# Kernel optimization log

Measured on AMD Instinct MI355X. Metric: run time of the kernel, lower is better.

## Reference

```python
import jax, jax.numpy as jnp
import numpy as np
from math import factorial

LMAX = 4
N_COEFF = (LMAX + 1) ** 2      # 25 real spherical-harmonic coefficients
N_RADII = 300                  # distance_bins
N_NODES = 512
FEAT = 128
RES_BETA, RES_ALPHA = 180, 360
DIST_STEP = 0.05


def _sh_basis(lmax, y, alpha):
    """Real spherical harmonics evaluated on a (beta, alpha) product grid.
    y = cos(beta) quadrature nodes. Returns [res_beta, res_alpha, (lmax+1)^2]."""
    B, A = len(y), len(alpha)
    P = np.zeros((lmax + 1, lmax + 1, B))
    P[0, 0] = 1.0
    s = np.sqrt(np.clip(1.0 - y * y, 0.0, None))
    for m in range(1, lmax + 1):
        P[m, m] = -(2 * m - 1) * s * P[m - 1, m - 1]
    for m in range(lmax):
        P[m + 1, m] = (2 * m + 1) * y * P[m, m]
    for m in range(lmax + 1):
        for l in range(m + 2, lmax + 1):
            P[l, m] = ((2 * l - 1) * y * P[l - 1, m] - (l + m - 1) * P[l - 2, m]) / (l - m)
    cols = []
    for l in range(lmax + 1):
        for m in range(-l, l + 1):
            am = abs(m)
            Nlm = np.sqrt((2 * l + 1) / (4 * np.pi) * factorial(l - am) / factorial(l + am))
            if m == 0:
                col = Nlm * P[l, 0][:, None] * np.ones((1, A))
            elif m > 0:
                col = np.sqrt(2.0) * Nlm * P[l, m][:, None] * np.cos(m * alpha)[None, :]
            else:
                col = np.sqrt(2.0) * Nlm * P[l, am][:, None] * np.sin(am * alpha)[None, :]
            cols.append(col)
    return np.stack(cols, axis=-1).astype(np.float32)


def setup_inputs() -> dict:
    key = jax.random.key(0)
    ks = jax.random.split(key, 14)

    def lin(k, a, b):
        return jax.random.normal(k, (a, b), jnp.float32) / np.float32(np.sqrt(a))

    x = jax.random.normal(ks[0], (N_NODES, FEAT), jnp.float32)
    fd = [FEAT, 128, 128, 64, 16, 2]
    td = [FEAT, 128, 128, 128, 128, 128, 6]
    fW = [lin(ks[1 + i], fd[i], fd[i + 1]) for i in range(5)]
    tW = [lin(ks[6 + i], td[i], td[i + 1]) for i in range(6)]
    pos_w = lin(ks[12], 2 * FEAT, N_RADII * N_COEFF)
    type_emb = jax.random.normal(ks[13], (5, FEAT), jnp.float32)

    y_np, w_np = np.polynomial.legendre.leggauss(RES_BETA)
    alpha_np = np.linspace(0.0, 2.0 * np.pi, RES_ALPHA, endpoint=False)
    basis = jnp.asarray(_sh_basis(LMAX, y_np, alpha_np))          # [B, A, C]
    qw = jnp.asarray(w_np / 2.0, jnp.float32)                     # gausslegendre / 2
    y_grid = jnp.asarray(y_np, jnp.float32)
    alpha_grid = jnp.asarray(alpha_np, jnp.float32)

    return {
        "x": x,
        "focus_w1": fW[0], "focus_w2": fW[1], "focus_w3": fW[2], "focus_w4": fW[3], "focus_w5": fW[4],
        "type_w1": tW[0], "type_w2": tW[1], "type_w3": tW[2], "type_w4": tW[3], "type_w5": tW[4], "type_w6": tW[5],
        "pos_w": pos_w, "type_emb": type_emb,
        "basis": basis, "qw": qw, "y_grid": y_grid, "alpha_grid": alpha_grid,
        "res_beta": RES_BETA, "res_alpha": RES_ALPHA,
    }


def reference(x, focus_w1, focus_w2, focus_w3, focus_w4, focus_w5,
              type_w1, type_w2, type_w3, type_w4, type_w5, type_w6,
              pos_w, type_emb, basis, qw, y_grid, alpha_grid,
              res_beta, res_alpha):
    n_nodes = x.shape[0]

    # --- focus MLP (relu), per-node logits; STOP logit 0 appended ---
    h = x
    for W in (focus_w1, focus_w2, focus_w3, focus_w4):
        h = jax.nn.relu(h @ W)
    focus_scores = (h @ focus_w5)[:, 0]                             # [n_nodes]
    focus_probs = jax.nn.softmax(jnp.concatenate([focus_scores, jnp.zeros((1,), x.dtype)]))
    focus = jnp.minimum(jnp.argmax(focus_probs), n_nodes - 1)

    # --- type MLP (softplus) on the focus node's features ---
    feat_f = x[focus]                                               # [128]
    th = feat_f
    for W in (type_w1, type_w2, type_w3, type_w4, type_w5):
        th = jax.nn.softplus(th @ W)
    type_dist = jax.nn.softmax(th @ type_w6)                        # [6]
    type_idx = jnp.minimum(jnp.argmax(type_dist), 4)

    # --- position head: SH coefficients per radial shell ---
    pos_in = jnp.concatenate([feat_f, type_emb[type_idx]])          # [256]
    coeffs = (pos_in @ pos_w).reshape(N_RADII, N_COEFF)             # [R, C]

    # to_s2grid: log-density on the sphere for every radial shell
    f = jnp.einsum('rc,bac->rba', coeffs, basis)                    # [R, B, A]
    log_meas = jnp.log(qw)[:, None] + jnp.log(2.0 * jnp.pi / res_alpha)  # [B, 1]

    # radial distribution: integral of exp(f) over the sphere, per shell
    log_radial = jax.nn.logsumexp(f + log_meas[None], axis=(1, 2))  # [R]
    radial_probs = jax.nn.softmax(log_radial)

    key = jax.random.key(42)
    k_r, k_a = jax.random.split(key)
    r_idx = jax.random.categorical(k_r, log_radial)

    # angular distribution at the sampled radius, normalized on S2
    fr = f[r_idx]                                                   # [B, A]
    logZr = jax.nn.logsumexp(fr + log_meas)
    angular_dist = jnp.exp(fr - logZr)                              # [B, A]

    joint_log = (fr + log_meas - logZr).reshape(-1)
    idx = jax.random.categorical(k_a, joint_log)
    y_i = idx // res_alpha
    a_i = idx % res_alpha

    radius_pred = (r_idx.astype(jnp.float32) + 1.0) * DIST_STEP
    return (type_dist, radial_probs, angular_dist, radius_pred, y_grid[y_i], alpha_grid[a_i])
```

## Files before the change

kernel.cpp:

```cpp
#include <hip/hip_runtime.h>
#include <math.h>
#include <stdint.h>

#define NNODES 512
#define FEAT   128
#define NR     300
#define NC     25
#define NB     180
#define NA     360
#define RSPLIT 4
#define BCHUNK (NB / RSPLIT)
#define O_TYPE   0
#define O_RAD    6
#define O_ANG    306
#define O_RADIUS 65106
#define O_Y      65107
#define O_ALPHA  65108

#define WS_KEYS   0
#define WS_TYPEI  5
#define WS_DEAD   8
#define WS_SCORES 320
#define WS_PV     840
#define WS_PI     1020
#define WS_Q      1664
#define WS_CXF    6176
#define WS_CEM    13696
#define WS_LRP    51200

#define G1_MLP   64
#define G1_PREP  18
#define G1_PFT   21
#define G1_PFP   240
#define G1_TOTAL (G1_MLP + G1_PREP + G1_PFT + G1_PFP)

__constant__ int c_m_of_c[25] = {0,-1,0,1,-2,-1,0,1,2,-3,-2,-1,0,1,2,3,-4,-3,-2,-1,0,1,2,3,4};
__constant__ int c_h_cnt[9] = {5,4,3,2,1,4,3,2,1};
__constant__ int c_h_idx[9][5] = {
  {0,2,6,12,20},
  {3,7,13,21,0},
  {8,14,22,0,0},
  {15,23,0,0,0},
  {24,0,0,0,0},
  {1,5,11,19,0},
  {4,10,18,0,0},
  {9,17,0,0,0},
  {16,0,0,0,0}};

__device__ __forceinline__ void tf2x32(uint32_t k0, uint32_t k1, uint32_t x0, uint32_t x1,
                                       uint32_t& o0, uint32_t& o1) {
  uint32_t ks2 = k0 ^ k1 ^ 0x1BD11BDAu;
#define TF_RND(r) { x0 += x1; x1 = (x1 << r) | (x1 >> (32 - r)); x1 ^= x0; }
  x0 += k0; x1 += k1;
  TF_RND(13) TF_RND(15) TF_RND(26) TF_RND(6)
  x0 += k1; x1 += ks2 + 1u;
  TF_RND(17) TF_RND(29) TF_RND(16) TF_RND(24)
  x0 += ks2; x1 += k0 + 2u;
  TF_RND(13) TF_RND(15) TF_RND(26) TF_RND(6)
  x0 += k0; x1 += k1 + 3u;
  TF_RND(17) TF_RND(29) TF_RND(16) TF_RND(24)
  x0 += k1; x1 += ks2 + 4u;
  TF_RND(13) TF_RND(15) TF_RND(26) TF_RND(6)
  x0 += ks2; x1 += k0 + 5u;
#undef TF_RND
  o0 = x0; o1 = x1;
}

__device__ __forceinline__ float gumbel32(uint32_t k0, uint32_t k1, uint32_t lo) {
  uint32_t o0, o1; tf2x32(k0, k1, 0u, lo, o0, o1);
  uint32_t bits = o0 ^ o1;
  float u = __uint_as_float((bits >> 9) | 0x3f800000u) - 1.0f;
  u = fmaxf(u, 1.1754944e-38f);
  return -logf(-logf(u));
}

__device__ __forceinline__ float softplusf(float s) {
  return fmaxf(s, 0.f) + log1pf(expf(-fabsf(s)));
}

__global__ __launch_bounds__(256) void k_front(const float* __restrict__ x,
    const float* __restrict__ w1, const float* __restrict__ w2, const float* __restrict__ w3,
    const float* __restrict__ w4, const float* __restrict__ w5,
    const float* __restrict__ basis, const float* __restrict__ alpha_grid,
    const float* __restrict__ tw1, const float* __restrict__ tw2, const float* __restrict__ tw3,
    const float* __restrict__ tw4, const float* __restrict__ tw5, const float* __restrict__ tw6,
    const float* __restrict__ pos_w,
    float* __restrict__ wsf) {
  __shared__ float A[8][128];
  __shared__ float B[8][128];
  int bx = blockIdx.x, t = threadIdx.x;

  if (bx < G1_MLP) {
    int base = bx * 8;
    for (int i = t; i < 8 * 128; i += 256) A[i >> 7][i & 127] = x[(base + (i >> 7)) * FEAT + (i & 127)];
    __syncthreads();
    int j = t & 127, h = t >> 7;
    {
      float a0 = 0, a1 = 0, a2 = 0, a3 = 0;
#pragma unroll 8
      for (int k = 0; k < 128; k++) {
        float wv = w1[k * 128 + j];
        a0 += A[h * 4 + 0][k] * wv; a1 += A[h * 4 + 1][k] * wv;
        a2 += A[h * 4 + 2][k] * wv; a3 += A[h * 4 + 3][k] * wv;
      }
      __syncthreads();
      B[h * 4 + 0][j] = fmaxf(a0, 0.f); B[h * 4 + 1][j] = fmaxf(a1, 0.f);
      B[h * 4 + 2][j] = fmaxf(a2, 0.f); B[h * 4 + 3][j] = fmaxf(a3, 0.f);
      __syncthreads();
    }
    {
      float a0 = 0, a1 = 0, a2 = 0, a3 = 0;
#pragma unroll 8
      for (int k = 0; k < 128; k++) {
        float wv = w2[k * 128 + j];
        a0 += B[h * 4 + 0][k] * wv; a1 += B[h * 4 + 1][k] * wv;
        a2 += B[h * 4 + 2][k] * wv; a3 += B[h * 4 + 3][k] * wv;
      }
      __syncthreads();
      A[h * 4 + 0][j] = fmaxf(a0, 0.f); A[h * 4 + 1][j] = fmaxf(a1, 0.f);
      A[h * 4 + 2][j] = fmaxf(a2, 0.f); A[h * 4 + 3][j] = fmaxf(a3, 0.f);
      __syncthreads();
    }
    {
      int j3 = t & 63, g = t >> 6;
      float a0 = 0, a1 = 0;
#pragma unroll 8
      for (int k = 0; k < 128; k++) {
        float wv = w3[k * 64 + j3];
        a0 += A[g * 2 + 0][k] * wv; a1 += A[g * 2 + 1][k] * wv;
      }
      __syncthreads();
      B[g * 2 + 0][j3] = fmaxf(a0, 0.f); B[g * 2 + 1][j3] = fmaxf(a1, 0.f);
      __syncthreads();
    }
    {
      int j4 = t & 15, g4 = t >> 4;
      if (g4 < 8) {
        float a0 = 0;
#pragma unroll
        for (int k = 0; k < 64; k++) a0 += B[g4][k] * w4[k * 16 + j4];
        A[g4][j4] = fmaxf(a0, 0.f);
      }
      __syncthreads();
    }
    if (t < 8) {
      float a0 = 0;
#pragma unroll
      for (int k = 0; k < 16; k++) a0 += A[t][k] * w5[k * 2 + 0];
      wsf[WS_SCORES + base + t] = a0;
    }
  } else if (bx < G1_MLP + G1_PREP) {
    int p = (bx - G1_MLP) * 256 + t;
    if (bx == G1_MLP && t == 0) {
      uint32_t* wu = (uint32_t*)wsf;
      uint32_t o0, o1;
      tf2x32(0u, 42u, 0u, 0u, o0, o1); wu[WS_KEYS + 0] = o0; wu[WS_KEYS + 1] = o1;
      tf2x32(0u, 42u, 0u, 1u, o0, o1); wu[WS_KEYS + 2] = o0; wu[WS_KEYS + 3] = o1;
    }
    if (p < NB * NC) {
      int b = p / NC, c = p % NC;
      int m = c_m_of_c[c];
      float q;
      if (m >= 0) {
        q = basis[(b * NA + 0) * NC + c];
      } else {
        float a10 = alpha_grid[10];
        q = basis[(b * NA + 10) * NC + c] / sinf((float)(-m) * a10);
      }
      wsf[WS_Q + p] = q;
    }
  } else if (bx < G1_MLP + G1_PREP + G1_PFT) {
    const float4* mats[5] = {(const float4*)tw1, (const float4*)tw2, (const float4*)tw3,
                             (const float4*)tw4, (const float4*)tw5};
    int lid = (bx - (G1_MLP + G1_PREP)) * 256 + t;
    float acc = 0.f;
    for (int vi = lid; vi < 20672; vi += G1_PFT * 256) {
      int mi = vi >> 12;
      float4 v;
      if (mi < 5) v = mats[mi][vi & 4095];
      else        v = ((const float4*)tw6)[vi - 20480];
      acc += v.x + v.y + v.z + v.w;
    }
    if (acc == -1.2345678e30f) wsf[WS_DEAD] = acc;
  } else {
    int lid = (bx - (G1_MLP + G1_PREP + G1_PFT)) * 256 + t;
    const float4* p4 = (const float4*)pos_w;
    float acc = 0.f;
    for (int i = lid; i < NR * NC * 256 / 4; i += G1_PFP * 256) {
      float4 v = p4[i];
      acc += v.x + v.y + v.z + v.w;
    }
    if (acc == -1.2345678e30f) wsf[WS_DEAD] = acc;
  }
}

__global__ __launch_bounds__(1024) void k_mid(const float* __restrict__ x,
    const float* __restrict__ w1, const float* __restrict__ w2, const float* __restrict__ w3,
    const float* __restrict__ w4, const float* __restrict__ w5, const float* __restrict__ w6,
    const float* __restrict__ type_emb, const float* __restrict__ pos_w,
    float* __restrict__ out, float* __restrict__ wsf) {
  __shared__ float wrv[16]; __shared__ int wri[16];
  __shared__ int f_sh;
  int t = threadIdx.x;
  int lane = t & 63, wid = t >> 6;
  float bv = -INFINITY; int bi = 1 << 30;
  if (t < NNODES + 1) { bv = (t < NNODES) ? wsf[WS_SCORES + t] : 0.f; bi = t; }
  for (int off = 32; off; off >>= 1) {
    float v2 = __shfl_down(bv, off); int i2 = __shfl_down(bi, off);
    if (v2 > bv || (v2 == bv && i2 < bi)) { bv = v2; bi = i2; }
  }
  if (lane == 0) { wrv[wid] = bv; wri[wid] = bi; }
  __syncthreads();
  if (t == 0) {
    float v0 = wrv[0]; int i0 = wri[0];
    for (int w = 1; w < 16; w++)
      if (wrv[w] > v0 || (wrv[w] == v0 && wri[w] < i0)) { v0 = wrv[w]; i0 = wri[w]; }
    f_sh = (i0 < NNODES - 1) ? i0 : (NNODES - 1);
  }
  __syncthreads();
  int focus = f_sh;

  if (blockIdx.x == 0) {
    __shared__ float src[128];
    __shared__ float partial[8][128];
    __shared__ float lg[6];
    if (t < 128) src[t] = x[focus * FEAT + t];
    __syncthreads();
    const float* Ws[5] = {w1, w2, w3, w4, w5};
#pragma unroll
    for (int L = 0; L < 5; L++) {
      const float* W = Ws[L];
      int j = t & 127, kc = t >> 7;
      float acc = 0.f;
#pragma unroll
      for (int k = 0; k < 16; k++) acc += src[kc * 16 + k] * W[(kc * 16 + k) * 128 + j];
      partial[kc][j] = acc;
      __syncthreads();
      if (t < 128) {
        float s = 0.f;
#pragma unroll
        for (int q = 0; q < 8; q++) s += partial[q][t];
        src[t] = softplusf(s);
      }
      __syncthreads();
    }
    float prod = 0.f;
    if (t < 768) { int o = t >> 7, j = t & 127; prod = src[j] * w6[j * 6 + o]; }
    for (int off = 32; off; off >>= 1) prod += __shfl_down(prod, off);
    if (t < 768 && lane == 0) wrv[wid] = prod;
    __syncthreads();
    if (t == 0) {
      for (int o = 0; o < 6; o++) lg[o] = wrv[2 * o] + wrv[2 * o + 1];
      float M = lg[0]; int am = 0;
      for (int i = 1; i < 6; i++) if (lg[i] > M) { M = lg[i]; am = i; }
      float e[6], S = 0.f;
      for (int i = 0; i < 6; i++) { e[i] = expf(lg[i] - M); S += e[i]; }
      for (int i = 0; i < 6; i++) out[O_TYPE + i] = e[i] / S;
      ((int*)wsf)[WS_TYPEI] = (am < 4) ? am : 4;
    }
  } else {
    __shared__ float xf[128];
    __shared__ float es[5 * 128];
    __shared__ float px[16][64];
    __shared__ float pe[5][16][64];
    if (t < 128) xf[t] = x[focus * FEAT + t];
    if (t < 640) es[t] = type_emb[t];
    __syncthreads();
    int oL = t & 63, kc = t >> 6;
    int o = (blockIdx.x - 1) * 64 + oL;
    bool valid = o < NR * NC;
    float ax = 0.f, e0 = 0.f, e1 = 0.f, e2 = 0.f, e3 = 0.f, e4 = 0.f;
    if (valid) {
#pragma unroll
      for (int k8 = 0; k8 < 8; k8++) {
        int k = kc * 8 + k8;
        float w0 = pos_w[k * (NR * NC) + o];
        ax += xf[k] * w0;
        float wv = pos_w[(128 + k) * (NR * NC) + o];
        e0 += es[k] * wv;        e1 += es[128 + k] * wv;
        e2 += es[256 + k] * wv;  e3 += es[384 + k] * wv;
        e4 += es[512 + k] * wv;
      }
    }
    px[kc][oL] = ax;
    pe[0][kc][oL] = e0; pe[1][kc][oL] = e1; pe[2][kc][oL] = e2;
    pe[3][kc][oL] = e3; pe[4][kc][oL] = e4;
    __syncthreads();
    if (t < 64) {
      int oo = (blockIdx.x - 1) * 64 + t;
      if (oo < NR * NC) {
        float s = 0.f;
#pragma unroll
        for (int q = 0; q < 16; q++) s += px[q][t];
        wsf[WS_CXF + oo] = s;
#pragma unroll
        for (int ti = 0; ti < 5; ti++) {
          float s2 = 0.f;
#pragma unroll
          for (int q = 0; q < 16; q++) s2 += pe[ti][q][t];
          wsf[WS_CEM + ti * (NR * NC) + oo] = s2;
        }
      }
    }
  }
}

__global__ __launch_bounds__(384) void k_radial_lse(const float* __restrict__ qw,
    const float* __restrict__ alpha_grid, float* __restrict__ wsf) {
  __shared__ float4 Hs4[BCHUNK * 3];
  __shared__ float cs[NC];
  __shared__ float wred[6];
  int bx = blockIdx.x;
  int r = bx >> 2, s = bx & 3;
  int b0 = s * BCHUNK;
  int t = threadIdx.x;
  float* Hs = (float*)Hs4;
  int ti = ((const int*)wsf)[WS_TYPEI];
  if (t < NC) cs[t] = wsf[WS_CXF + r * NC + t] + wsf[WS_CEM + ti * (NR * NC) + r * NC + t];
  __syncthreads();
  const float LOGM = -4.0482054576f;
  for (int p = t; p < BCHUNK * 9; p += 384) {
    int b = p / 9, jj = p % 9;
    int bg = b0 + b;
    int n = c_h_cnt[jj];
    float acc = 0.f;
    for (int q = 0; q < n; q++) { int c = c_h_idx[jj][q]; acc += cs[c] * wsf[WS_Q + bg * NC + c]; }
    if (jj == 0) acc += logf(qw[bg]) + LOGM;
    Hs[b * 12 + jj] = acc;
  }
  __syncthreads();
  float c1 = 0, c2 = 0, c3 = 0, c4 = 0, s1 = 0, s2 = 0, s3 = 0, s4 = 0;
  bool act = t < NA;
  if (act) {
    float al = alpha_grid[t];
    sincosf(al, &s1, &c1);
    sincosf(2.f * al, &s2, &c2);
    sincosf(3.f * al, &s3, &c3);
    sincosf(4.f * al, &s4, &c4);
  }
  float acc = 0.f;
#pragma unroll 5
  for (int b = 0; b < BCHUNK; b++) {
    float4 h0 = Hs4[b * 3 + 0], h1 = Hs4[b * 3 + 1], h2 = Hs4[b * 3 + 2];
    float f = h0.x + h0.y * c1 + h0.z * c2 + h0.w * c3 + h1.x * c4
            + h1.y * s1 + h1.z * s2 + h1.w * s3 + h2.x * s4;
    acc += act ? __expf(f) : 0.f;
  }
  for (int off = 32; off; off >>= 1) acc += __shfl_down(acc, off);
  int wid = t >> 6, lane = t & 63;
  if (lane == 0) wred[wid] = acc;
  __syncthreads();
  if (t == 0) {
    float ss = 0.f;
    for (int w = 0; w < 6; w++) ss += wred[w];
    wsf[WS_LRP + bx] = ss;
  }
}

__global__ __launch_bounds__(384) void k_ang(const float* __restrict__ qw,
    const float* __restrict__ alpha_grid, float* __restrict__ out, float* __restrict__ wsf) {
  __shared__ float wred[6]; __shared__ int wri[6];
  __shared__ float fss[NR];
  __shared__ float cs[NC];
  __shared__ float hsh[12];
  __shared__ float S_sh; __shared__ int r_sh;
  int b = blockIdx.x, t = threadIdx.x;
  int lane = t & 63, wid = t >> 6;
  const uint32_t* wu = (const uint32_t*)wsf;
  uint32_t kr0 = wu[WS_KEYS + 0], kr1 = wu[WS_KEYS + 1];
  uint32_t ka0 = wu[WS_KEYS + 2], ka1 = wu[WS_KEYS + 3];
  int ti = ((const int*)wsf)[WS_TYPEI];

  float sv = 0.f, lr = -INFINITY;
  if (t < NR) {
    sv = wsf[WS_LRP + 4 * t] + wsf[WS_LRP + 4 * t + 1]
       + wsf[WS_LRP + 4 * t + 2] + wsf[WS_LRP + 4 * t + 3];
    fss[t] = sv;
    lr = logf(sv);
  }
  float ss = sv;
  for (int off = 32; off; off >>= 1) ss += __shfl_down(ss, off);
  if (lane == 0) wred[wid] = ss;
  __syncthreads();
  if (t == 0) {
    float S = 0.f;
    for (int w = 0; w < 6; w++) S += wred[w];
    S_sh = S;
  }
  __syncthreads();
  if (b == 0 && t < NR) out[O_RAD + t] = sv / S_sh;
  float v = (t < NR) ? lr + gumbel32(kr0, kr1, (uint32_t)t) : -INFINITY;
  int bi = (t < NR) ? t : (1 << 30);
  for (int off = 32; off; off >>= 1) {
    float v2 = __shfl_down(v, off); int i2 = __shfl_down(bi, off);
    if (v2 > v || (v2 == v && i2 < bi)) { v = v2; bi = i2; }
  }
  __syncthreads();
  if (lane == 0) { wred[wid] = v; wri[wid] = bi; }
  __syncthreads();
  if (t == 0) {
    float v0 = wred[0]; int i0 = wri[0];
    for (int w = 1; w < 6; w++)
      if (wred[w] > v0 || (wred[w] == v0 && wri[w] < i0)) { v0 = wred[w]; i0 = wri[w]; }
    r_sh = i0;
    if (b == 0) out[O_RADIUS] = (float)(i0 + 1) * 0.05f;
  }
  __syncthreads();
  int r = r_sh;
  float invZ = 1.0f / fss[r];

  if (t < NC) cs[t] = wsf[WS_CXF + r * NC + t] + wsf[WS_CEM + ti * (NR * NC) + r * NC + t];
  __syncthreads();
  if (t < 9) {
    int n = c_h_cnt[t];
    float acc = 0.f;
    for (int q = 0; q < n; q++) { int c = c_h_idx[t][q]; acc += cs[c] * wsf[WS_Q + b * NC + c]; }
    hsh[t] = acc;
  }
  __syncthreads();
  const float MEAS = 0.01745329252f;
  float elm = qw[b] * MEAS;
  float lm = logf(elm);
  float va = -INFINITY; int idx = (t < NA) ? b * NA + t : (1 << 30);
  if (t < NA) {
    float al = alpha_grid[t];
    float s1, c1, s2, c2, s3, c3, s4, c4;
    sincosf(al, &s1, &c1); sincosf(2.f * al, &s2, &c2);
    sincosf(3.f * al, &s3, &c3); sincosf(4.f * al, &s4, &c4);
    float f = hsh[0] + hsh[1] * c1 + hsh[2] * c2 + hsh[3] * c3 + hsh[4] * c4
            + hsh[5] * s1 + hsh[6] * s2 + hsh[7] * s3 + hsh[8] * s4;
    out[O_ANG + idx] = __expf(f) * invZ;
    va = f + lm + gumbel32(ka0, ka1, (uint32_t)idx);
  }
  for (int off = 32; off; off >>= 1) {
    float v2 = __shfl_down(va, off); int i2 = __shfl_down(idx, off);
    if (v2 > va || (v2 == va && i2 < idx)) { va = v2; idx = i2; }
  }
  __syncthreads();
  if (lane == 0) { wred[wid] = va; wri[wid] = idx; }
  __syncthreads();
  if (t == 0) {
    float v0 = wred[0]; int i0 = wri[0];
    for (int w = 1; w < 6; w++)
      if (wred[w] > v0 || (wred[w] == v0 && wri[w] < i0)) { v0 = wred[w]; i0 = wri[w]; }
    wsf[WS_PV + b] = v0;
    ((int*)wsf)[WS_PI + b] = i0;
  }
}

__global__ __launch_bounds__(256) void k_ang_final(const float* __restrict__ y_grid,
    const float* __restrict__ alpha_grid, float* __restrict__ out, float* __restrict__ wsf) {
  __shared__ float wr[4]; __shared__ int wi[4];
  int t = threadIdx.x, lane = t & 63, wid = t >> 6;
  float v = (t < NB) ? wsf[WS_PV + t] : -INFINITY;
  int i = (t < NB) ? ((const int*)wsf)[WS_PI + t] : (1 << 30);
  for (int off = 32; off; off >>= 1) {
    float v2 = __shfl_down(v, off); int i2 = __shfl_down(i, off);
    if (v2 > v || (v2 == v && i2 < i)) { v = v2; i = i2; }
  }
  if (lane == 0) { wr[wid] = v; wi[wid] = i; }
  __syncthreads();
  if (t == 0) {
    float v0 = wr[0]; int i0 = wi[0];
    for (int w = 1; w < 4; w++)
      if (wr[w] > v0 || (wr[w] == v0 && wi[w] < i0)) { v0 = wr[w]; i0 = wi[w]; }
    int yi = i0 / NA, ai = i0 % NA;
    out[O_Y] = y_grid[yi];
    out[O_ALPHA] = alpha_grid[ai];
  }
}

extern "C" void kernel_launch(void* const* d_in, const int* in_sizes, int n_in,
                              void* d_out, int out_size, void* d_ws, size_t ws_size,
                              hipStream_t stream) {
  const float* x          = (const float*)d_in[0];
  const float* fw1        = (const float*)d_in[1];
  const float* fw2        = (const float*)d_in[2];
  const float* fw3        = (const float*)d_in[3];
  const float* fw4        = (const float*)d_in[4];
  const float* fw5        = (const float*)d_in[5];
  const float* tw1        = (const float*)d_in[6];
  const float* tw2        = (const float*)d_in[7];
  const float* tw3        = (const float*)d_in[8];
  const float* tw4        = (const float*)d_in[9];
  const float* tw5        = (const float*)d_in[10];
  const float* tw6        = (const float*)d_in[11];
  const float* pos_w      = (const float*)d_in[12];
  const float* type_emb   = (const float*)d_in[13];
  const float* basis      = (const float*)d_in[14];
  const float* qw         = (const float*)d_in[15];
  const float* y_grid     = (const float*)d_in[16];
  const float* alpha_grid = (const float*)d_in[17];
  (void)in_sizes; (void)n_in; (void)out_size; (void)ws_size;
  float* out = (float*)d_out;
  float* wsf = (float*)d_ws;

  k_front<<<G1_TOTAL, 256, 0, stream>>>(x, fw1, fw2, fw3, fw4, fw5, basis, alpha_grid,
                                        tw1, tw2, tw3, tw4, tw5, tw6, pos_w, wsf);
  k_mid<<<1 + (NR * NC + 63) / 64, 1024, 0, stream>>>(x, tw1, tw2, tw3, tw4, tw5, tw6,
                                                      type_emb, pos_w, out, wsf);
  k_radial_lse<<<NR * RSPLIT, 384, 0, stream>>>(qw, alpha_grid, wsf);
  k_ang<<<NB, 384, 0, stream>>>(qw, alpha_grid, out, wsf);
  k_ang_final<<<1, 256, 0, stream>>>(y_grid, alpha_grid, out, wsf);
}
```

Baseline: 54.44 us.

## Move type-embedding projection to front kernel and fuse final argmax via atomics

The five type-embedding projections of pos_w's second half move from k_mid into new k_front blocks, replacing the pure prefetch blocks, so k_mid only computes the focus-feature projection. The final angular argmax kernel is removed: each k_ang block atomically maxes a packed (ordered value, inverted index) key and the last block, found with an atomic counter, writes the sampled y/alpha. This cuts one launch and shortens k_mid's critical path, at the cost of atomics, and it relies on k_radial_lse resetting the counters each run.

Measured after the change: 56.35 us. 3.5% more time.

```diff
diff --git a/kernel.cpp b/kernel.cpp
--- a/kernel.cpp
+++ b/kernel.cpp
@@ -20,9 +20,9 @@
 #define WS_KEYS   0
 #define WS_TYPEI  5
 #define WS_DEAD   8
+#define WS_AKEY   16
+#define WS_ACNT   18
 #define WS_SCORES 320
-#define WS_PV     840
-#define WS_PI     1020
 #define WS_Q      1664
 #define WS_CXF    6176
 #define WS_CEM    13696
@@ -31,8 +31,8 @@
 #define G1_MLP   64
 #define G1_PREP  18
 #define G1_PFT   21
-#define G1_PFP   240
-#define G1_TOTAL (G1_MLP + G1_PREP + G1_PFT + G1_PFP)
+#define G1_CEM   118
+#define G1_TOTAL (G1_MLP + G1_PREP + G1_PFT + G1_CEM)
 
 __constant__ int c_m_of_c[25] = {0,-1,0,1,-2,-1,0,1,2,-3,-2,-1,0,1,2,3,-4,-3,-2,-1,0,1,2,3,4};
 __constant__ int c_h_cnt[9] = {5,4,3,2,1,4,3,2,1};
@@ -84,7 +84,7 @@
     const float* __restrict__ basis, const float* __restrict__ alpha_grid,
     const float* __restrict__ tw1, const float* __restrict__ tw2, const float* __restrict__ tw3,
     const float* __restrict__ tw4, const float* __restrict__ tw5, const float* __restrict__ tw6,
-    const float* __restrict__ pos_w,
+    const float* __restrict__ pos_w, const float* __restrict__ type_emb,
     float* __restrict__ wsf) {
   __shared__ float A[8][128];
   __shared__ float B[8][128];
@@ -183,21 +183,44 @@
     }
     if (acc == -1.2345678e30f) wsf[WS_DEAD] = acc;
   } else {
-    int lid = (bx - (G1_MLP + G1_PREP + G1_PFT)) * 256 + t;
-    const float4* p4 = (const float4*)pos_w;
-    float acc = 0.f;
-    for (int i = lid; i < NR * NC * 256 / 4; i += G1_PFP * 256) {
-      float4 v = p4[i];
-      acc += v.x + v.y + v.z + v.w;
-    }
-    if (acc == -1.2345678e30f) wsf[WS_DEAD] = acc;
+    __shared__ float es[5 * 128];
+    __shared__ float part[5][4][64];
+    int cb = bx - (G1_MLP + G1_PREP + G1_PFT);
+    for (int i = t; i < 640; i += 256) es[i] = type_emb[i];
+    __syncthreads();
+    int oL = t & 63, kc = t >> 6;
+    int o = cb * 64 + oL;
+    float e0 = 0, e1 = 0, e2 = 0, e3 = 0, e4 = 0;
+    if (o < NR * NC) {
+#pragma unroll 8
+      for (int k8 = 0; k8 < 32; k8++) {
+        int k = kc * 32 + k8;
+        float wv = pos_w[(128 + k) * (NR * NC) + o];
+        e0 += es[k] * wv;        e1 += es[128 + k] * wv;
+        e2 += es[256 + k] * wv;  e3 += es[384 + k] * wv;
+        e4 += es[512 + k] * wv;
+      }
+    }
+    part[0][kc][oL] = e0; part[1][kc][oL] = e1; part[2][kc][oL] = e2;
+    part[3][kc][oL] = e3; part[4][kc][oL] = e4;
+    __syncthreads();
+    if (t < 64) {
+      int oo = cb * 64 + t;
+      if (oo < NR * NC) {
+#pragma unroll
+        for (int ti = 0; ti < 5; ti++) {
+          float s = part[ti][0][t] + part[ti][1][t] + part[ti][2][t] + part[ti][3][t];
+          wsf[WS_CEM + ti * (NR * NC) + oo] = s;
+        }
+      }
+    }
   }
 }
 
 __global__ __launch_bounds__(1024) void k_mid(const float* __restrict__ x,
     const float* __restrict__ w1, const float* __restrict__ w2, const float* __restrict__ w3,
     const float* __restrict__ w4, const float* __restrict__ w5, const float* __restrict__ w6,
-    const float* __restrict__ type_emb, const float* __restrict__ pos_w,
+    const float* __restrict__ pos_w,
     float* __restrict__ out, float* __restrict__ wsf) {
   __shared__ float wrv[16]; __shared__ int wri[16];
   __shared__ int f_sh;
@@ -250,6 +273,7 @@
     if (t < 768 && lane == 0) wrv[wid] = prod;
     __syncthreads();
     if (t == 0) {
+      float lg[6];
       for (int o = 0; o < 6; o++) lg[o] = wrv[2 * o] + wrv[2 * o + 1];
       float M = lg[0]; int am = 0;
       for (int i = 1; i < 6; i++) if (lg[i] > M) { M = lg[i]; am = i; }
@@ -260,31 +284,20 @@
     }
   } else {
     __shared__ float xf[128];
-    __shared__ float es[5 * 128];
     __shared__ float px[16][64];
-    __shared__ float pe[5][16][64];
     if (t < 128) xf[t] = x[focus * FEAT + t];
-    if (t < 640) es[t] = type_emb[t];
     __syncthreads();
     int oL = t & 63, kc = t >> 6;
     int o = (blockIdx.x - 1) * 64 + oL;
-    bool valid = o < NR * NC;
-    float ax = 0.f, e0 = 0.f, e1 = 0.f, e2 = 0.f, e3 = 0.f, e4 = 0.f;
-    if (valid) {
+    float ax = 0.f;
+    if (o < NR * NC) {
 #pragma unroll
       for (int k8 = 0; k8 < 8; k8++) {
         int k = kc * 8 + k8;
-        float w0 = pos_w[k * (NR * NC) + o];
-        ax += xf[k] * w0;
-        float wv = pos_w[(128 + k) * (NR * NC) + o];
-        e0 += es[k] * wv;        e1 += es[128 + k] * wv;
-        e2 += es[256 + k] * wv;  e3 += es[384 + k] * wv;
-        e4 += es[512 + k] * wv;
+        ax += xf[k] * pos_w[k * (NR * NC) + o];
       }
     }
     px[kc][oL] = ax;
-    pe[0][kc][oL] = e0; pe[1][kc][oL] = e1; pe[2][kc][oL] = e2;
-    pe[3][kc][oL] = e3; pe[4][kc][oL] = e4;
     __syncthreads();
     if (t < 64) {
       int oo = (blockIdx.x - 1) * 64 + t;
@@ -293,13 +306,6 @@
 #pragma unroll
         for (int q = 0; q < 16; q++) s += px[q][t];
         wsf[WS_CXF + oo] = s;
-#pragma unroll
-        for (int ti = 0; ti < 5; ti++) {
-          float s2 = 0.f;
-#pragma unroll
-          for (int q = 0; q < 16; q++) s2 += pe[ti][q][t];
-          wsf[WS_CEM + ti * (NR * NC) + oo] = s2;
-        }
       }
     }
   }
@@ -315,6 +321,10 @@
   int b0 = s * BCHUNK;
   int t = threadIdx.x;
   float* Hs = (float*)Hs4;
+  if (bx == 0 && t == 0) {
+    *(unsigned long long*)(wsf + WS_AKEY) = 0ULL;
+    *(unsigned int*)(wsf + WS_ACNT) = 0u;
+  }
   int ti = ((const int*)wsf)[WS_TYPEI];
   if (t < NC) cs[t] = wsf[WS_CXF + r * NC + t] + wsf[WS_CEM + ti * (NR * NC) + r * NC + t];
   __syncthreads();
@@ -358,7 +368,8 @@
 }
 
 __global__ __launch_bounds__(384) void k_ang(const float* __restrict__ qw,
-    const float* __restrict__ alpha_grid, float* __restrict__ out, float* __restrict__ wsf) {
+    const float* __restrict__ alpha_grid, const float* __restrict__ y_grid,
+    float* __restrict__ out, float* __restrict__ wsf) {
   __shared__ float wred[6]; __shared__ int wri[6];
   __shared__ float fss[NR];
   __shared__ float cs[NC];
@@ -443,30 +454,21 @@
     float v0 = wred[0]; int i0 = wri[0];
     for (int w = 1; w < 6; w++)
       if (wred[w] > v0 || (wred[w] == v0 && wri[w] < i0)) { v0 = wred[w]; i0 = wri[w]; }
-    wsf[WS_PV + b] = v0;
-    ((int*)wsf)[WS_PI + b] = i0;
-  }
-}
-
-__global__ __launch_bounds__(256) void k_ang_final(const float* __restrict__ y_grid,
-    const float* __restrict__ alpha_grid, float* __restrict__ out, float* __restrict__ wsf) {
-  __shared__ float wr[4]; __shared__ int wi[4];
-  int t = threadIdx.x, lane = t & 63, wid = t >> 6;
-  float v = (t < NB) ? wsf[WS_PV + t] : -INFINITY;
-  int i = (t < NB) ? ((const int*)wsf)[WS_PI + t] : (1 << 30);
-  for (int off = 32; off; off >>= 1) {
-    float v2 = __shfl_down(v, off); int i2 = __shfl_down(i, off);
-    if (v2 > v || (v2 == v && i2 < i)) { v = v2; i = i2; }
-  }
-  if (lane == 0) { wr[wid] = v; wi[wid] = i; }
-  __syncthreads();
-  if (t == 0) {
-    float v0 = wr[0]; int i0 = wi[0];
-    for (int w = 1; w < 4; w++)
-      if (wr[w] > v0 || (wr[w] == v0 && wi[w] < i0)) { v0 = wr[w]; i0 = wi[w]; }
-    int yi = i0 / NA, ai = i0 % NA;
-    out[O_Y] = y_grid[yi];
-    out[O_ALPHA] = alpha_grid[ai];
+    uint32_t u = __float_as_uint(v0);
+    uint32_t ordv = (u & 0x80000000u) ? ~u : (u | 0x80000000u);
+    unsigned long long key = ((unsigned long long)ordv << 32)
+                           | (unsigned long long)(0xFFFFFFFFu - (uint32_t)i0);
+    atomicMax((unsigned long long*)(wsf + WS_AKEY), key);
+    __threadfence();
+    unsigned int old = atomicAdd((unsigned int*)(wsf + WS_ACNT), 1u);
+    if (old == NB - 1) {
+      __threadfence();
+      unsigned long long kk = atomicMax((unsigned long long*)(wsf + WS_AKEY), 0ULL);
+      uint32_t gidx = 0xFFFFFFFFu - (uint32_t)(kk & 0xFFFFFFFFull);
+      int yi = (int)(gidx / NA), ai = (int)(gidx % NA);
+      out[O_Y] = y_grid[yi];
+      out[O_ALPHA] = alpha_grid[ai];
+    }
   }
 }
 
@@ -496,10 +498,9 @@
   float* wsf = (float*)d_ws;
 
   k_front<<<G1_TOTAL, 256, 0, stream>>>(x, fw1, fw2, fw3, fw4, fw5, basis, alpha_grid,
-                                        tw1, tw2, tw3, tw4, tw5, tw6, pos_w, wsf);
+                                        tw1, tw2, tw3, tw4, tw5, tw6, pos_w, type_emb, wsf);
   k_mid<<<1 + (NR * NC + 63) / 64, 1024, 0, stream>>>(x, tw1, tw2, tw3, tw4, tw5, tw6,
-                                                      type_emb, pos_w, out, wsf);
+                                                      pos_w, out, wsf);
   k_radial_lse<<<NR * RSPLIT, 384, 0, stream>>>(qw, alpha_grid, wsf);
-  k_ang<<<NB, 384, 0, stream>>>(qw, alpha_grid, out, wsf);
-  k_ang_final<<<1, 256, 0, stream>>>(y_grid, alpha_grid, out, wsf);
-}
+  k_ang<<<NB, 384, 0, stream>>>(qw, alpha_grid, y_grid, out, wsf);
+}
```
